# Kernel optimization log

Hardware: AMD Instinct MI355X
Metric: run time of the kernel (lower is better)

## Reference

```python
import jax, jax.numpy as jnp
from jax import lax
import numpy as np

B, D, L = 32, 64, 4096
E = 8          # num_experts
K = 2          # top-k
OC = 32        # out_channels


def setup_inputs() -> dict:
    key = jax.random.key(0)
    ks = jax.random.split(key, 6)
    x = jax.random.normal(ks[0], (B, D, L), dtype=jnp.float32)
    # gating weight [D*5, E] (torch init is zeros; use small random for a meaningful reference)
    w_gate = jax.random.normal(ks[1], (D * 5, E), dtype=jnp.float32) * 0.02
    # Conv1d(D -> OC, kernel 3)
    conv1_w = jax.random.normal(ks[2], (OC, D, 3), dtype=jnp.float32) * (1.0 / np.sqrt(D * 3))
    conv1_b = jax.random.normal(ks[3], (OC,), dtype=jnp.float32) * 0.01
    # Conv1d(OC -> OC*E, kernel 1)
    conv2_w = jax.random.normal(ks[4], (OC * E, OC, 1), dtype=jnp.float32) * (1.0 / np.sqrt(OC))
    conv2_b = jax.random.normal(ks[5], (OC * E,), dtype=jnp.float32) * 0.01
    return {"x": x, "w_gate": w_gate, "conv1_w": conv1_w, "conv1_b": conv1_b,
            "conv2_w": conv2_w, "conv2_b": conv2_b}


def _gates(g_in, w_gate):
    # eval-mode noisy_top_k_gating: no noise, softmax -> top-(k+1) -> renormalize top-k -> scatter
    logits = jax.nn.softmax(g_in @ w_gate, axis=1)            # [B, E]
    top_v, top_i = lax.top_k(logits, min(K + 1, E))           # sorted descending
    vk = top_v[:, :K]
    ik = top_i[:, :K]
    gk = vk / (jnp.sum(vk, axis=1, keepdims=True) + 1e-6)
    gates = jnp.zeros_like(logits).at[jnp.arange(logits.shape[0])[:, None], ik].set(gk)
    return gates


def reference(x, w_gate, conv1_w, conv1_b, conv2_w, conv2_b):
    b, d, l = x.shape
    g_in = x[:, :, -6:-1].reshape(b, d * 5)                   # last-5-timestep gating features
    gates = _gates(g_in, w_gate)                              # [B, E]
    dn = ("NCH", "OIH", "NCH")
    h = lax.conv_general_dilated(x, conv1_w, (1,), "VALID", dimension_numbers=dn)
    h = jnp.tanh(h + conv1_b[None, :, None])                  # [B, OC, L-2]
    out = lax.conv_general_dilated(h, conv2_w, (1,), "VALID", dimension_numbers=dn)
    out = out + conv2_b[None, :, None]                        # [B, OC*E, L']
    lp = out.shape[-1]
    out = out.transpose(0, 2, 1).reshape(b, lp, OC, E)        # [B, L', OC, E]
    moe = jnp.einsum("blde,be->bld", out, gates)              # weighted combine
    return moe.transpose(0, 2, 1)                             # [B, OC, L']
```

## Files before the change

### kernel.cpp

```cpp
#include <hip/hip_runtime.h>
#include <math.h>

#define B_  32
#define D_  64
#define L_  4096
#define E_  8
#define OC_ 32
#define LP_ 4094

typedef __attribute__((ext_vector_type(8)))  short short8;
typedef __attribute__((ext_vector_type(16))) float float16;

static __device__ __forceinline__ unsigned short f2bf(float f) {
    unsigned u = __float_as_uint(f);
    return (unsigned short)((u + 0x7fffu + ((u >> 16) & 1u)) >> 16);
}
static __device__ __forceinline__ unsigned cvtpk(float a, float b) {
    unsigned r;
    asm("v_cvt_pk_bf16_f32 %0, %1, %2" : "=v"(r) : "v"(a), "v"(b));
    return r;
}
static __device__ __forceinline__ float fast_tanh(float x) {
    float e = __expf(2.0f * x);
    return fmaf(-2.0f, __builtin_amdgcn_rcpf(e + 1.0f), 1.0f);
}

__global__ __launch_bounds__(256)
void prep_kernel(const float* __restrict__ x,
                 const float* __restrict__ w_gate,
                 const float* __restrict__ c1w,
                 const float* __restrict__ c2w,
                 const float* __restrict__ c2b,
                 float* __restrict__ beff,
                 unsigned short* __restrict__ aF,
                 unsigned short* __restrict__ wf2)
{
    const int tid = threadIdx.x;

    if (blockIdx.x == 8) {
        for (int i = tid; i < 12 * 64 * 8; i += 256) {
            int ks = i >> 9, lane = (i >> 3) & 63, ii = i & 7;
            int oc = lane & 31, half = lane >> 5;
            int kp = ks * 16 + half * 8 + ii;
            int t = kp >> 6, c = kp & 63;
            aF[i] = f2bf(c1w[oc * 192 + c * 3 + t]);
        }
        return;
    }

    const int wv = tid >> 6, lane = tid & 63;
    const int b  = blockIdx.x * 4 + wv;
    const int d  = lane;

    float xv[5];
    #pragma unroll
    for (int t = 0; t < 5; ++t)
        xv[t] = x[((size_t)b * D_ + d) * L_ + (L_ - 6) + t];

    float part[E_];
    #pragma unroll
    for (int e = 0; e < E_; ++e) part[e] = 0.f;
    #pragma unroll
    for (int t = 0; t < 5; ++t) {
        const float* wg = w_gate + (d * 5 + t) * E_;
        #pragma unroll
        for (int e = 0; e < E_; ++e) part[e] += xv[t] * wg[e];
    }
    #pragma unroll
    for (int off = 1; off < 64; off <<= 1) {
        #pragma unroll
        for (int e = 0; e < E_; ++e)
            part[e] += __shfl_xor(part[e], off, 64);
    }
    float m = part[0];
    #pragma unroll
    for (int e = 1; e < E_; ++e) m = fmaxf(m, part[e]);
    float p[E_], s = 0.f;
    #pragma unroll
    for (int e = 0; e < E_; ++e) { p[e] = expf(part[e] - m); s += p[e]; }
    float inv = 1.f / s;
    #pragma unroll
    for (int e = 0; e < E_; ++e) p[e] *= inv;

    int i0 = 0;
    #pragma unroll
    for (int e = 1; e < E_; ++e) if (p[e] > p[i0]) i0 = e;
    int i1 = (i0 == 0) ? 1 : 0;
    #pragma unroll
    for (int e = 0; e < E_; ++e) {
        if (e == i0) continue;
        if (p[e] > p[i1]) i1 = e;
    }
    const float v0 = p[i0], v1 = p[i1];
    const float den = v0 + v1 + 1e-6f;
    const float g0 = v0 / den, g1 = v1 / den;

    {
        const int dd = lane & 31, half = lane >> 5;
        #pragma unroll
        for (int ks = 0; ks < 2; ++ks) {
            #pragma unroll
            for (int i = 0; i < 8; ++i) {
                int oc = ks * 16 + half * 8 + i;
                float v = g0 * c2w[(dd * E_ + i0) * OC_ + oc]
                        + g1 * c2w[(dd * E_ + i1) * OC_ + oc];
                wf2[((b * 2 + ks) * 64 + lane) * 8 + i] = f2bf(v);
            }
        }
    }
    if (d < OC_)
        beff[b * OC_ + d] = g0 * c2b[d * E_ + i0] + g1 * c2b[d * E_ + i1];
}

static __device__ __forceinline__ void compute_tile(
    const unsigned short* __restrict__ xbuf,
    const short8* a1, const short8* a2,
    const float* __restrict__ c1b,
    const float* __restrict__ be,
    float* __restrict__ outb,
    int l0, int wv, int cl, int hi)
{
    const int cb = wv * 32;
    float16 acc = (float16)0.0f;
    #pragma unroll
    for (int t = 0; t < 3; ++t) {
        int row = cb + cl + t;
        int rb  = row * 128;
        int swz = (row & 7) << 4;
        #pragma unroll
        for (int q = 0; q < 4; ++q) {
            int off = (rb + q * 32 + hi * 16) ^ swz;
            short8 bf = *(const short8*)((const char*)xbuf + off);
            acc = __builtin_amdgcn_mfma_f32_32x32x16_bf16(a1[t * 4 + q], bf, acc, 0, 0, 0);
        }
    }

    float th[16];
    #pragma unroll
    for (int r = 0; r < 16; ++r) {
        int row = (r & 3) + 8 * (r >> 2) + 4 * hi;
        th[r] = fast_tanh(acc[r] + c1b[row]);
    }

    unsigned x0a = hi ? cvtpk(th[0],  th[1])  : cvtpk(th[4],  th[5]);
    unsigned x0b = hi ? cvtpk(th[2],  th[3])  : cvtpk(th[6],  th[7]);
    unsigned x1a = hi ? cvtpk(th[8],  th[9])  : cvtpk(th[12], th[13]);
    unsigned x1b = hi ? cvtpk(th[10], th[11]) : cvtpk(th[14], th[15]);
    unsigned r0a = (unsigned)__shfl_xor((int)x0a, 32, 64);
    unsigned r0b = (unsigned)__shfl_xor((int)x0b, 32, 64);
    unsigned r1a = (unsigned)__shfl_xor((int)x1a, 32, 64);
    unsigned r1b = (unsigned)__shfl_xor((int)x1b, 32, 64);

    union U { short8 s8; unsigned u[4]; };
    U b0, b1;
    b0.u[0] = hi ? r0a : cvtpk(th[0], th[1]);
    b0.u[1] = hi ? r0b : cvtpk(th[2], th[3]);
    b0.u[2] = hi ? cvtpk(th[4], th[5]) : r0a;
    b0.u[3] = hi ? cvtpk(th[6], th[7]) : r0b;
    b1.u[0] = hi ? r1a : cvtpk(th[8], th[9]);
    b1.u[1] = hi ? r1b : cvtpk(th[10], th[11]);
    b1.u[2] = hi ? cvtpk(th[12], th[13]) : r1a;
    b1.u[3] = hi ? cvtpk(th[14], th[15]) : r1b;

    float16 acc2 = (float16)0.0f;
    acc2 = __builtin_amdgcn_mfma_f32_32x32x16_bf16(a2[0], b0.s8, acc2, 0, 0, 0);
    acc2 = __builtin_amdgcn_mfma_f32_32x32x16_bf16(a2[1], b1.s8, acc2, 0, 0, 0);

    int l = l0 + cb + cl;
    if (l < LP_) {
        float* ob = outb + l;
        #pragma unroll
        for (int r = 0; r < 16; ++r) {
            int row = (r & 3) + 8 * (r >> 2) + 4 * hi;
            ob[(size_t)row * LP_] = acc2[r] + be[row];
        }
    }
}

__global__ __launch_bounds__(512, 2)
void fused_main(const float* __restrict__ x,
                const unsigned short* __restrict__ aF,
                const unsigned short* __restrict__ wf2,
                const float* __restrict__ beff,
                const float* __restrict__ c1b,
                float* __restrict__ out)
{
    __shared__ __align__(16) unsigned short xT0[260 * 64];
    __shared__ __align__(16) unsigned short xT1[260 * 64];

    const int tid  = threadIdx.x;
    const int lane = tid & 63;
    const int wv   = tid >> 6;
    const int b    = blockIdx.x >> 3;
    const int S    = (blockIdx.x & 7) << 9;
    const float* xb = x + (size_t)b * (D_ * L_);

    const int c2 = tid >> 4;
    const int jb = (tid & 15) << 2;
    const float* p0 = xb + (size_t)(2 * c2) * L_;
    const float* p1 = p0 + L_;
    const int haloc = tid >> 1;
    const int haloj = tid & 1;

    float4 A0[4], A1[4];
    #pragma unroll
    for (int jq = 0; jq < 4; ++jq) {
        int j = S + jq * 64 + jb;
        A0[jq] = *(const float4*)(p0 + j);
        A1[jq] = *(const float4*)(p1 + j);
    }
    float hA0 = 0.f, hA1 = 0.f;
    if (tid < 64) {
        int lg = S + 256 + haloj;
        hA0 = xb[(size_t)(2 * haloc) * L_ + lg];
        hA1 = xb[(size_t)(2 * haloc + 1) * L_ + lg];
    }

    short8 a1[12];
    #pragma unroll
    for (int ks = 0; ks < 12; ++ks)
        a1[ks] = *(const short8*)(aF + (ks * 64 + lane) * 8);
    short8 a2[2];
    a2[0] = *(const short8*)(wf2 + ((b * 2 + 0) * 64 + lane) * 8);
    a2[1] = *(const short8*)(wf2 + ((b * 2 + 1) * 64 + lane) * 8);
    const float* be = beff + b * OC_;
    float* outb = out + (size_t)b * (OC_ * (size_t)LP_);

    const int cl = lane & 31;
    const int hi = lane >> 5;

    #pragma unroll
    for (int jq = 0; jq < 4; ++jq) {
        float e0[4] = {A0[jq].x, A0[jq].y, A0[jq].z, A0[jq].w};
        float e1[4] = {A1[jq].x, A1[jq].y, A1[jq].z, A1[jq].w};
        #pragma unroll
        for (int r = 0; r < 4; ++r) {
            int row = jq * 64 + jb + r;
            int off = (row * 128 + c2 * 4) ^ ((row & 7) << 4);
            *(unsigned*)((char*)xT0 + off) = cvtpk(e0[r], e1[r]);
        }
    }
    if (tid < 64) {
        int row = 256 + haloj;
        int off = (row * 128 + haloc * 4) ^ ((row & 7) << 4);
        *(unsigned*)((char*)xT0 + off) = cvtpk(hA0, hA1);
    }

    float4 B0[4], B1[4];
    #pragma unroll
    for (int jq = 0; jq < 4; ++jq) {
        int j = S + 256 + jq * 64 + jb;
        B0[jq] = *(const float4*)(p0 + j);
        B1[jq] = *(const float4*)(p1 + j);
    }
    float hB0 = 0.f, hB1 = 0.f;
    if (tid < 64) {
        int lg = S + 512 + haloj;
        if (lg > L_ - 1) lg = L_ - 1;
        hB0 = xb[(size_t)(2 * haloc) * L_ + lg];
        hB1 = xb[(size_t)(2 * haloc + 1) * L_ + lg];
    }

    __syncthreads();

    compute_tile(xT0, a1, a2, c1b, be, outb, S, wv, cl, hi);

    __syncthreads();

    #pragma unroll
    for (int jq = 0; jq < 4; ++jq) {
        float e0[4] = {B0[jq].x, B0[jq].y, B0[jq].z, B0[jq].w};
        float e1[4] = {B1[jq].x, B1[jq].y, B1[jq].z, B1[jq].w};
        #pragma unroll
        for (int r = 0; r < 4; ++r) {
            int row = jq * 64 + jb + r;
            int off = (row * 128 + c2 * 4) ^ ((row & 7) << 4);
            *(unsigned*)((char*)xT1 + off) = cvtpk(e0[r], e1[r]);
        }
    }
    if (tid < 64) {
        int row = 256 + haloj;
        int off = (row * 128 + haloc * 4) ^ ((row & 7) << 4);
        *(unsigned*)((char*)xT1 + off) = cvtpk(hB0, hB1);
    }

    __syncthreads();

    compute_tile(xT1, a1, a2, c1b, be, outb, S + 256, wv, cl, hi);
}

extern "C" void kernel_launch(void* const* d_in, const int* in_sizes, int n_in,
                              void* d_out, int out_size, void* d_ws, size_t ws_size,
                              hipStream_t stream)
{
    const float* x      = (const float*)d_in[0];
    const float* w_gate = (const float*)d_in[1];
    const float* c1w    = (const float*)d_in[2];
    const float* c1b    = (const float*)d_in[3];
    const float* c2w    = (const float*)d_in[4];
    const float* c2b    = (const float*)d_in[5];
    float* out = (float*)d_out;

    char* ws = (char*)d_ws;
    float* beff         = (float*)ws;
    unsigned short* aF  = (unsigned short*)(ws + 4096);
    unsigned short* wf2 = (unsigned short*)(ws + 16384);

    prep_kernel<<<9, 256, 0, stream>>>(x, w_gate, c1w, c2w, c2b, beff, aF, wf2);
    fused_main<<<B_ * 8, 512, 0, stream>>>(x, aF, wf2, beff, c1b, out);
}
```

Before: 22.75 us.

## Fuse gating and weight-prep kernel into main conv kernel, drop workspace round trip

Removes the separate prep kernel and instead has every block compute the softmax top-2 gating for its batch, build the gated conv2 weights in registers, and convert conv1 weights to bf16 fragments in shared memory. The effective bias is computed inline at store time. This eliminates one kernel launch and the dependency gap plus the workspace write/read, at the cost of redundant gating and weight conversion in all 8 blocks per batch. Launch bounds drop to 1 block per SM-hint, which may change occupancy.

```diff
diff --git a/kernel.cpp b/kernel.cpp
--- a/kernel.cpp
+++ b/kernel.cpp
@@ -11,10 +11,6 @@
 typedef __attribute__((ext_vector_type(8)))  short short8;
 typedef __attribute__((ext_vector_type(16))) float float16;
 
-static __device__ __forceinline__ unsigned short f2bf(float f) {
-    unsigned u = __float_as_uint(f);
-    return (unsigned short)((u + 0x7fffu + ((u >> 16) & 1u)) >> 16);
-}
 static __device__ __forceinline__ unsigned cvtpk(float a, float b) {
     unsigned r;
     asm("v_cvt_pk_bf16_f32 %0, %1, %2" : "=v"(r) : "v"(a), "v"(b));
@@ -25,98 +21,21 @@
     return fmaf(-2.0f, __builtin_amdgcn_rcpf(e + 1.0f), 1.0f);
 }
 
-__global__ __launch_bounds__(256)
-void prep_kernel(const float* __restrict__ x,
-                 const float* __restrict__ w_gate,
-                 const float* __restrict__ c1w,
-                 const float* __restrict__ c2w,
-                 const float* __restrict__ c2b,
-                 float* __restrict__ beff,
-                 unsigned short* __restrict__ aF,
-                 unsigned short* __restrict__ wf2)
-{
-    const int tid = threadIdx.x;
-
-    if (blockIdx.x == 8) {
-        for (int i = tid; i < 12 * 64 * 8; i += 256) {
-            int ks = i >> 9, lane = (i >> 3) & 63, ii = i & 7;
-            int oc = lane & 31, half = lane >> 5;
-            int kp = ks * 16 + half * 8 + ii;
-            int t = kp >> 6, c = kp & 63;
-            aF[i] = f2bf(c1w[oc * 192 + c * 3 + t]);
-        }
-        return;
-    }
-
-    const int wv = tid >> 6, lane = tid & 63;
-    const int b  = blockIdx.x * 4 + wv;
-    const int d  = lane;
-
-    float xv[5];
-    #pragma unroll
-    for (int t = 0; t < 5; ++t)
-        xv[t] = x[((size_t)b * D_ + d) * L_ + (L_ - 6) + t];
-
-    float part[E_];
-    #pragma unroll
-    for (int e = 0; e < E_; ++e) part[e] = 0.f;
-    #pragma unroll
-    for (int t = 0; t < 5; ++t) {
-        const float* wg = w_gate + (d * 5 + t) * E_;
-        #pragma unroll
-        for (int e = 0; e < E_; ++e) part[e] += xv[t] * wg[e];
-    }
-    #pragma unroll
-    for (int off = 1; off < 64; off <<= 1) {
-        #pragma unroll
-        for (int e = 0; e < E_; ++e)
-            part[e] += __shfl_xor(part[e], off, 64);
-    }
-    float m = part[0];
-    #pragma unroll
-    for (int e = 1; e < E_; ++e) m = fmaxf(m, part[e]);
-    float p[E_], s = 0.f;
-    #pragma unroll
-    for (int e = 0; e < E_; ++e) { p[e] = expf(part[e] - m); s += p[e]; }
-    float inv = 1.f / s;
-    #pragma unroll
-    for (int e = 0; e < E_; ++e) p[e] *= inv;
-
-    int i0 = 0;
-    #pragma unroll
-    for (int e = 1; e < E_; ++e) if (p[e] > p[i0]) i0 = e;
-    int i1 = (i0 == 0) ? 1 : 0;
-    #pragma unroll
-    for (int e = 0; e < E_; ++e) {
-        if (e == i0) continue;
-        if (p[e] > p[i1]) i1 = e;
-    }
-    const float v0 = p[i0], v1 = p[i1];
-    const float den = v0 + v1 + 1e-6f;
-    const float g0 = v0 / den, g1 = v1 / den;
-
-    {
-        const int dd = lane & 31, half = lane >> 5;
-        #pragma unroll
-        for (int ks = 0; ks < 2; ++ks) {
-            #pragma unroll
-            for (int i = 0; i < 8; ++i) {
-                int oc = ks * 16 + half * 8 + i;
-                float v = g0 * c2w[(dd * E_ + i0) * OC_ + oc]
-                        + g1 * c2w[(dd * E_ + i1) * OC_ + oc];
-                wf2[((b * 2 + ks) * 64 + lane) * 8 + i] = f2bf(v);
-            }
-        }
-    }
-    if (d < OC_)
-        beff[b * OC_ + d] = g0 * c2b[d * E_ + i0] + g1 * c2b[d * E_ + i1];
-}
+__global__ __launch_bounds__(512, 1)
+void fused_all(const float* __restrict__ x,
+               const float* __restrict__ w_gate,
+               const float* __restrict__ c1w,
+               const float* __restrict__ c1b,
+               const float* __restrict__ c2w,
+               const float* __restrict__ c2b,
+               float* __restrict__ out);
 
 static __device__ __forceinline__ void compute_tile(
     const unsigned short* __restrict__ xbuf,
     const short8* a1, const short8* a2,
     const float* __restrict__ c1b,
-    const float* __restrict__ be,
+    const float* __restrict__ c2b,
+    int i0, int i1, float g0, float g1,
     float* __restrict__ outb,
     int l0, int wv, int cl, int hi)
 {
@@ -172,21 +91,24 @@
         #pragma unroll
         for (int r = 0; r < 16; ++r) {
             int row = (r & 3) + 8 * (r >> 2) + 4 * hi;
-            ob[(size_t)row * LP_] = acc2[r] + be[row];
-        }
-    }
-}
-
-__global__ __launch_bounds__(512, 2)
-void fused_main(const float* __restrict__ x,
-                const unsigned short* __restrict__ aF,
-                const unsigned short* __restrict__ wf2,
-                const float* __restrict__ beff,
-                const float* __restrict__ c1b,
-                float* __restrict__ out)
+            float bb = fmaf(g0, c2b[row * E_ + i0], g1 * c2b[row * E_ + i1]);
+            ob[(size_t)row * LP_] = acc2[r] + bb;
+        }
+    }
+}
+
+__global__ __launch_bounds__(512, 1)
+void fused_all(const float* __restrict__ x,
+               const float* __restrict__ w_gate,
+               const float* __restrict__ c1w,
+               const float* __restrict__ c1b,
+               const float* __restrict__ c2w,
+               const float* __restrict__ c2b,
+               float* __restrict__ out)
 {
     __shared__ __align__(16) unsigned short xT0[260 * 64];
     __shared__ __align__(16) unsigned short xT1[260 * 64];
+    __shared__ __align__(16) unsigned short aFl[12 * 64 * 8];
 
     const int tid  = threadIdx.x;
     const int lane = tid & 63;
@@ -216,18 +138,100 @@
         hA1 = xb[(size_t)(2 * haloc + 1) * L_ + lg];
     }
 
-    short8 a1[12];
-    #pragma unroll
-    for (int ks = 0; ks < 12; ++ks)
-        a1[ks] = *(const short8*)(aF + (ks * 64 + lane) * 8);
-    short8 a2[2];
-    a2[0] = *(const short8*)(wf2 + ((b * 2 + 0) * 64 + lane) * 8);
-    a2[1] = *(const short8*)(wf2 + ((b * 2 + 1) * 64 + lane) * 8);
-    const float* be = beff + b * OC_;
-    float* outb = out + (size_t)b * (OC_ * (size_t)LP_);
+    const int w_oc = tid >> 4;
+    const int w_c0 = (tid & 15) << 2;
+    float wv12[12];
+    {
+        const float* wp = c1w + w_oc * 192 + w_c0 * 3;
+        *(float4*)(wv12 + 0) = *(const float4*)(wp + 0);
+        *(float4*)(wv12 + 4) = *(const float4*)(wp + 4);
+        *(float4*)(wv12 + 8) = *(const float4*)(wp + 8);
+    }
+
+    int i0, i1;
+    float g0, g1;
+    {
+        const int d = lane;
+        float part[E_];
+        #pragma unroll
+        for (int e = 0; e < E_; ++e) part[e] = 0.f;
+        #pragma unroll
+        for (int t = 0; t < 5; ++t) {
+            float xvt = xb[(size_t)d * L_ + (L_ - 6) + t];
+            const float* wgp = w_gate + (d * 5 + t) * E_;
+            float4 wa = *(const float4*)wgp;
+            float4 wb = *(const float4*)(wgp + 4);
+            part[0] = fmaf(xvt, wa.x, part[0]);
+            part[1] = fmaf(xvt, wa.y, part[1]);
+            part[2] = fmaf(xvt, wa.z, part[2]);
+            part[3] = fmaf(xvt, wa.w, part[3]);
+            part[4] = fmaf(xvt, wb.x, part[4]);
+            part[5] = fmaf(xvt, wb.y, part[5]);
+            part[6] = fmaf(xvt, wb.z, part[6]);
+            part[7] = fmaf(xvt, wb.w, part[7]);
+        }
+        #pragma unroll
+        for (int off = 1; off < 64; off <<= 1) {
+            #pragma unroll
+            for (int e = 0; e < E_; ++e)
+                part[e] += __shfl_xor(part[e], off, 64);
+        }
+        float m = part[0];
+        #pragma unroll
+        for (int e = 1; e < E_; ++e) m = fmaxf(m, part[e]);
+        float p[E_], s = 0.f;
+        #pragma unroll
+        for (int e = 0; e < E_; ++e) { p[e] = expf(part[e] - m); s += p[e]; }
+        float inv = 1.f / s;
+        #pragma unroll
+        for (int e = 0; e < E_; ++e) p[e] *= inv;
+
+        i0 = 0;
+        #pragma unroll
+        for (int e = 1; e < E_; ++e) if (p[e] > p[i0]) i0 = e;
+        i1 = (i0 == 0) ? 1 : 0;
+        #pragma unroll
+        for (int e = 0; e < E_; ++e) {
+            if (e == i0) continue;
+            if (p[e] > p[i1]) i1 = e;
+        }
+        const float v0 = p[i0], v1 = p[i1];
+        const float den = v0 + v1 + 1e-6f;
+        g0 = v0 / den;
+        g1 = v1 / den;
+    }
 
     const int cl = lane & 31;
     const int hi = lane >> 5;
+
+    short8 a2[2];
+    #pragma unroll
+    for (int ks = 0; ks < 2; ++ks) {
+        const float* q0 = c2w + (cl * E_ + i0) * OC_ + ks * 16 + hi * 8;
+        const float* q1 = c2w + (cl * E_ + i1) * OC_ + ks * 16 + hi * 8;
+        float4 u0a = *(const float4*)q0, u0b = *(const float4*)(q0 + 4);
+        float4 u1a = *(const float4*)q1, u1b = *(const float4*)(q1 + 4);
+        union { short8 s8; unsigned u[4]; } f;
+        f.u[0] = cvtpk(fmaf(g0, u0a.x, g1 * u1a.x), fmaf(g0, u0a.y, g1 * u1a.y));
+        f.u[1] = cvtpk(fmaf(g0, u0a.z, g1 * u1a.z), fmaf(g0, u0a.w, g1 * u1a.w));
+        f.u[2] = cvtpk(fmaf(g0, u0b.x, g1 * u1b.x), fmaf(g0, u0b.y, g1 * u1b.y));
+        f.u[3] = cvtpk(fmaf(g0, u0b.z, g1 * u1b.z), fmaf(g0, u0b.w, g1 * u1b.w));
+        a2[ks] = f.s8;
+    }
+
+    {
+        const int ksoff = w_c0 >> 4;
+        const int half  = (w_c0 >> 3) & 1;
+        const int ii0   = w_c0 & 7;
+        #pragma unroll
+        for (int t = 0; t < 3; ++t) {
+            unsigned u0 = cvtpk(wv12[0 * 3 + t], wv12[1 * 3 + t]);
+            unsigned u1 = cvtpk(wv12[2 * 3 + t], wv12[3 * 3 + t]);
+            int base = ((t * 4 + ksoff) * 64 + half * 32 + w_oc) * 8 + ii0;
+            uint2 w2 = {u0, u1};
+            *(uint2*)(aFl + base) = w2;
+        }
+    }
 
     #pragma unroll
     for (int jq = 0; jq < 4; ++jq) {
@@ -263,7 +267,14 @@
 
     __syncthreads();
 
-    compute_tile(xT0, a1, a2, c1b, be, outb, S, wv, cl, hi);
+    short8 a1[12];
+    #pragma unroll
+    for (int ks = 0; ks < 12; ++ks)
+        a1[ks] = *(const short8*)(aFl + (ks * 64 + lane) * 8);
+
+    float* outb = out + (size_t)b * (OC_ * (size_t)LP_);
+
+    compute_tile(xT0, a1, a2, c1b, c2b, i0, i1, g0, g1, outb, S, wv, cl, hi);
 
     __syncthreads();
 
@@ -286,7 +297,7 @@
 
     __syncthreads();
 
-    compute_tile(xT1, a1, a2, c1b, be, outb, S + 256, wv, cl, hi);
+    compute_tile(xT1, a1, a2, c1b, c2b, i0, i1, g0, g1, outb, S + 256, wv, cl, hi);
 }
 
 extern "C" void kernel_launch(void* const* d_in, const int* in_sizes, int n_in,
@@ -301,11 +312,5 @@
     const float* c2b    = (const float*)d_in[5];
     float* out = (float*)d_out;
 
-    char* ws = (char*)d_ws;
-    float* beff         = (float*)ws;
-    unsigned short* aF  = (unsigned short*)(ws + 4096);
-    unsigned short* wf2 = (unsigned short*)(ws + 16384);
-
-    prep_kernel<<<9, 256, 0, stream>>>(x, w_gate, c1w, c2w, c2b, beff, aF, wf2);
-    fused_main<<<B_ * 8, 512, 0, stream>>>(x, aF, wf2, beff, c1b, out);
-}
+    fused_all<<<B_ * 8, 512, 0, stream>>>(x, w_gate, c1w, c1b, c2w, c2b, out);
+}
```

After: 20.71 us. -9.0%, faster.
